# Kernel optimization log

Hardware: AMD Instinct MI355X
Metric: run time of the kernel (lower is better)

The kernel has to match this reference:

```python
import jax, jax.numpy as jnp
import numpy as np

B, S, D = 2, 2048, 2048
H, KVH, HD = 16, 4, 128
REP = H // KVH  # 4
THETA = 10000.0


def setup_inputs() -> dict:
    key = jax.random.key(0)
    ks = jax.random.split(key, 5)
    scale = 0.02
    x = jax.random.normal(ks[0], (B, S, D), dtype=jnp.float32)
    Wq = jax.random.normal(ks[1], (D, H * HD), dtype=jnp.float32) * scale
    Wk = jax.random.normal(ks[2], (D, KVH * HD), dtype=jnp.float32) * scale
    Wv = jax.random.normal(ks[3], (D, KVH * HD), dtype=jnp.float32) * scale
    Wo = jax.random.normal(ks[4], (H * HD, D), dtype=jnp.float32) * scale
    return {"x": x, "Wq": Wq, "Wk": Wk, "Wv": Wv, "Wo": Wo}


def _rope_cos_sin(seq_len, dtype):
    # HF-style rotary embedding: inv_freq over even dims, duplicated halves
    inv_freq = 1.0 / (THETA ** (jnp.arange(0, HD, 2, dtype=jnp.float32) / HD))
    pos = jnp.arange(seq_len, dtype=jnp.float32)
    ang = pos[:, None] * inv_freq[None, :]          # [S, HD/2]
    emb = jnp.concatenate([ang, ang], axis=-1)       # [S, HD]
    return jnp.cos(emb).astype(dtype), jnp.sin(emb).astype(dtype)


def _rotate_half(t):
    t1, t2 = jnp.split(t, 2, axis=-1)
    return jnp.concatenate([-t2, t1], axis=-1)


def reference(x, Wq, Wk, Wv, Wo):
    bsz, seq_len, _ = x.shape
    q = (x @ Wq).reshape(bsz, seq_len, H, HD).transpose(0, 2, 1, 3)    # [B,H,S,HD]
    k = (x @ Wk).reshape(bsz, seq_len, KVH, HD).transpose(0, 2, 1, 3)  # [B,KVH,S,HD]
    v = (x @ Wv).reshape(bsz, seq_len, KVH, HD).transpose(0, 2, 1, 3)
    cos, sin = _rope_cos_sin(seq_len, q.dtype)       # [S,HD]
    cos = cos[None, None, :, :]
    sin = sin[None, None, :, :]
    q = q * cos + _rotate_half(q) * sin
    k = k * cos + _rotate_half(k) * sin
    # repeat_interleave KV heads to match Q heads
    k = jnp.repeat(k, REP, axis=1)                   # [B,H,S,HD]
    v = jnp.repeat(v, REP, axis=1)
    scores = jnp.einsum('bhqd,bhkd->bhqk', q, k) / jnp.sqrt(jnp.float32(HD)).astype(q.dtype)
    i = jnp.arange(seq_len)
    causal = jnp.where(i[None, :] > i[:, None], jnp.float32(-jnp.inf), 0.0).astype(scores.dtype)
    scores = scores + causal[None, None, :, :]
    probs = jax.nn.softmax(scores.astype(jnp.float32), axis=-1).astype(q.dtype)
    out = jnp.einsum('bhqk,bhkd->bhqd', probs, v)    # [B,H,S,HD]
    out = out.transpose(0, 2, 1, 3).reshape(bsz, seq_len, H * HD)
    return out @ Wo
```

## Files before the change

### kernel.cpp

```cpp
#include <hip/hip_runtime.h>
#include <math.h>

#define B_   2
#define S_   2048
#define D_   2048
#define H_   16
#define KVH_ 4
#define HD_  128
#define REP_ 4

typedef __attribute__((ext_vector_type(8))) short bf16x8;
typedef __attribute__((ext_vector_type(4))) short bf16x4;
typedef __attribute__((ext_vector_type(4))) float f32x4;

#define QSCALE_LOG2E 0.1275266977097153f

__device__ __forceinline__ unsigned short f2bf(float x) {
    union { float f; unsigned u; } v; v.f = x;
    unsigned r = v.u + 0x7FFF + ((v.u >> 16) & 1);
    return (unsigned short)(r >> 16);
}

__device__ __forceinline__ unsigned short f2bf_fast(float x) {
    union { float f; unsigned u; } v; v.f = x;
    return (unsigned short)((v.u + 0x8000) >> 16);
}

__device__ __forceinline__ void gl_lds16(const unsigned short* g, unsigned short* l) {
    __builtin_amdgcn_global_load_lds(
        (const __attribute__((address_space(1))) unsigned int*)g,
        (__attribute__((address_space(3))) unsigned int*)l,
        16, 0, 0);
}

#define PH_BAR() do { asm volatile("" ::: "memory"); \
                      __builtin_amdgcn_s_barrier();  \
                      asm volatile("" ::: "memory"); } while (0)
#define VMW6 asm volatile("s_waitcnt vmcnt(6)" ::: "memory")
#define VMW4 asm volatile("s_waitcnt vmcnt(4)" ::: "memory")
#define VMW0 asm volatile("s_waitcnt vmcnt(0)" ::: "memory")

__global__ void cast_bf16(const float* __restrict__ src,
                          unsigned short* __restrict__ dst, int n4)
{
    int i = blockIdx.x * 256 + threadIdx.x;
    if (i >= n4) return;
    float4 v = *(const float4*)&src[(size_t)i * 4];
    bf16x4 o;
    o[0] = (short)f2bf(v.x); o[1] = (short)f2bf(v.y);
    o[2] = (short)f2bf(v.z); o[3] = (short)f2bf(v.w);
    *(bf16x4*)&dst[(size_t)i * 4] = o;
}

__global__ __launch_bounds__(256) void cast_transpose_all(
    const float* __restrict__ Wq, const float* __restrict__ Wk,
    const float* __restrict__ Wv, const float* __restrict__ Wo,
    unsigned short* __restrict__ Wqt, unsigned short* __restrict__ Wkt,
    unsigned short* __restrict__ Wvt, unsigned short* __restrict__ Wot)
{
    __shared__ float T[32][33];
    const int y = blockIdx.y;
    const float* src; unsigned short* dst; int C, bj;
    if (y < 64)      { src = Wq; dst = Wqt; C = 2048; bj = y; }
    else if (y < 80) { src = Wk; dst = Wkt; C = 512;  bj = y - 64; }
    else if (y < 96) { src = Wv; dst = Wvt; C = 512;  bj = y - 80; }
    else             { src = Wo; dst = Wot; C = 2048; bj = y - 96; }

    const int bi = blockIdx.x;
    const int t  = threadIdx.x;
    const int r  = t >> 3, cq = (t & 7) * 4;

    float4 v = *(const float4*)&src[(size_t)(bi * 32 + r) * C + bj * 32 + cq];
    T[r][cq + 0] = v.x; T[r][cq + 1] = v.y;
    T[r][cq + 2] = v.z; T[r][cq + 3] = v.w;
    __syncthreads();

    bf16x4 o;
    o[0] = (short)f2bf(T[cq + 0][r]);
    o[1] = (short)f2bf(T[cq + 1][r]);
    o[2] = (short)f2bf(T[cq + 2][r]);
    o[3] = (short)f2bf(T[cq + 3][r]);
    *(bf16x4*)&dst[(size_t)(bj * 32 + r) * 2048 + bi * 32 + cq] = o;
}

__global__ __launch_bounds__(512, 2) void qkv_mfma8(
    const unsigned short* __restrict__ Ah,
    const unsigned short* __restrict__ Wqt,
    const unsigned short* __restrict__ Wkt,
    const unsigned short* __restrict__ Wvt,
    unsigned short* __restrict__ Qh, unsigned short* __restrict__ Kh,
    unsigned short* __restrict__ Vt)
{
    __shared__ __align__(16) unsigned short lds[65536];

    const int bid = blockIdx.x;
    const int swz = (bid & 7) * 24 + (bid >> 3);
    const int bm = swz / 12, bn = swz % 12;
    const int m0 = bm * 256, n0 = bn * 256;

    const int tid  = threadIdx.x;
    const int w    = tid >> 6;
    const int lane = tid & 63;
    const int lo16 = lane & 15, quad = lane >> 4;
    const int wm   = w >> 2, wn = w & 3;

    const unsigned short* Bt;
    if (n0 < 2048)      Bt = Wqt + (size_t)n0 * 2048;
    else if (n0 < 2560) Bt = Wkt + (size_t)(n0 - 2048) * 2048;
    else                Bt = Wvt + (size_t)(n0 - 2560) * 2048;
    const unsigned short* Ag   = Ah + (size_t)m0 * 2048;
    const unsigned short* AgH1 = Ag + (size_t)128 * 2048;
    const unsigned short* BtH1 = Bt + (size_t)128 * 2048;

    const int rs   = lane >> 3;
    const int sce  = (((lane & 7) ^ rs) << 3);
    const int grow = w * 8 + rs;

    #define STAGE(gb, k0, lb) do {                                          \
        const unsigned short* _g = (gb) + (size_t)grow * 2048 + (k0) + sce; \
        gl_lds16(_g,                     (lb) + w * 512);                   \
        gl_lds16(_g + (size_t)64 * 2048, (lb) + (8 + w) * 512);             \
    } while (0)

    const int swb = (lo16 & 7) << 4;
    const int ac0 = (quad << 4) ^ swb;
    const int ac1 = (64 | (quad << 4)) ^ swb;
    char* ldsb = (char*)lds;
    const int abase = (wm * 128 + lo16) * 128;
    const int bbase = (wn * 16 + lo16) * 128 + 32768;

    f32x4 acc[8][4];
    #pragma unroll
    for (int mf = 0; mf < 8; ++mf)
        #pragma unroll
        for (int j = 0; j < 4; ++j) acc[mf][j] = (f32x4){0.f, 0.f, 0.f, 0.f};

    bf16x8 a0[4][2], a1[4][2], b0[2][2], b1[2][2];

    #define MM(Aa, Bb, mo, jo)                                               \
        _Pragma("unroll") for (int mf = 0; mf < 4; ++mf)                     \
        _Pragma("unroll") for (int j = 0; j < 2; ++j) {                      \
            acc[(mo)+mf][(jo)+j] = __builtin_amdgcn_mfma_f32_16x16x32_bf16(  \
                Aa[mf][0], Bb[j][0], acc[(mo)+mf][(jo)+j], 0, 0, 0);         \
            acc[(mo)+mf][(jo)+j] = __builtin_amdgcn_mfma_f32_16x16x32_bf16(  \
                Aa[mf][1], Bb[j][1], acc[(mo)+mf][(jo)+j], 0, 0, 0);         \
        }

    STAGE(Bt,   0,  lds + 16384);
    STAGE(BtH1, 0,  lds + 24576);
    STAGE(Ag,   0,  lds + 0);
    STAGE(AgH1, 0,  lds + 8192);
    STAGE(Bt,   64, lds + 32768 + 16384);
    STAGE(BtH1, 64, lds + 32768 + 24576);
    STAGE(Ag,   64, lds + 32768);
    VMW6;
    PH_BAR();

    #define PHASES(p, t)                                                         \
    {   _Pragma("unroll") for (int mf = 0; mf < 4; ++mf) {                       \
            a0[mf][0] = *(const bf16x8*)(ldsb + (p)*65536 + abase + mf*2048 + ac0); \
            a0[mf][1] = *(const bf16x8*)(ldsb + (p)*65536 + abase + mf*2048 + ac1); \
        }                                                                        \
        _Pragma("unroll") for (int j = 0; j < 2; ++j) {                          \
            b0[j][0] = *(const bf16x8*)(ldsb + (p)*65536 + bbase + j*8192 + ac0); \
            b0[j][1] = *(const bf16x8*)(ldsb + (p)*65536 + bbase + j*8192 + ac1); \
        }                                                                        \
        STAGE(AgH1, ((t)+1)*64, lds + ((p)^1)*32768 + 8192);                     \
        PH_BAR(); __builtin_amdgcn_s_setprio(1);                                 \
        MM(a0, b0, 0, 0);                                                        \
        __builtin_amdgcn_s_setprio(0); PH_BAR();                                 \
        _Pragma("unroll") for (int j = 0; j < 2; ++j) {                          \
            b1[j][0] = *(const bf16x8*)(ldsb + (p)*65536 + bbase + (j+2)*8192 + ac0); \
            b1[j][1] = *(const bf16x8*)(ldsb + (p)*65536 + bbase + (j+2)*8192 + ac1); \
        }                                                                        \
        STAGE(Bt, ((t)+2)*64, lds + (p)*32768 + 16384);                          \
        PH_BAR(); __builtin_amdgcn_s_setprio(1);                                 \
        MM(a0, b1, 0, 2);                                                        \
        __builtin_amdgcn_s_setprio(0); PH_BAR();                                 \
        _Pragma("unroll") for (int mf = 0; mf < 4; ++mf) {                       \
            a1[mf][0] = *(const bf16x8*)(ldsb + (p)*65536 + abase + (mf+4)*2048 + ac0); \
            a1[mf][1] = *(const bf16x8*)(ldsb + (p)*65536 + abase + (mf+4)*2048 + ac1); \
        }                                                                        \
        STAGE(BtH1, ((t)+2)*64, lds + (p)*32768 + 24576);                        \
        PH_BAR(); __builtin_amdgcn_s_setprio(1);                                 \
        MM(a1, b0, 4, 0);                                                        \
        __builtin_amdgcn_s_setprio(0); PH_BAR();                                 \
        STAGE(Ag, ((t)+2)*64, lds + (p)*32768);                                  \
        PH_BAR(); __builtin_amdgcn_s_setprio(1);                                 \
        MM(a1, b1, 4, 2);                                                        \
        __builtin_amdgcn_s_setprio(0);                                           \
        VMW6;                                                                    \
        PH_BAR();                                                                \
    }

    for (int it = 0; it < 16; ++it) {
        const int t = 2 * it;
        PHASES(0, t);
        PHASES(1, t + 1);
    }

    VMW0;
    PH_BAR();

    const int bb = m0 >> 11;
    const int s0loc = m0 & 2047;

    if (n0 < 2560) {
        const bool isQ = (n0 < 2048);
        const int h0 = isQ ? (n0 >> 7) : ((n0 - 2048) >> 7);
        const float post = isQ ? QSCALE_LOG2E : 1.0f;
        unsigned short* db[2];
        #pragma unroll
        for (int hp = 0; hp < 2; ++hp)
            db[hp] = isQ
                ? Qh + (((size_t)bb * H_   + h0 + hp) * S_) * HD_
                : Kh + (((size_t)bb * KVH_ + h0 + hp) * S_) * HD_;
        const int d = wn * 16 + lo16;
        const float inv = exp2f(-(float)d * 0.20761871093344086f);
        #pragma unroll
        for (int mf = 0; mf < 8; ++mf) {
            #pragma unroll
            for (int r = 0; r < 4; ++r) {
                int s = s0loc + wm * 128 + mf * 16 + quad * 4 + r;
                float sn, c;
                sincosf((float)s * inv, &sn, &c);
                #pragma unroll
                for (int hp = 0; hp < 2; ++hp) {
                    float lo = acc[mf][2 * hp + 0][r];
                    float hi = acc[mf][2 * hp + 1][r];
                    unsigned short* drow = db[hp] + (size_t)s * HD_;
                    drow[d]      = f2bf((lo * c - hi * sn) * post);
                    drow[d + 64] = f2bf((hi * c + lo * sn) * post);
                }
            }
        }
    } else {
        const int g0 = (n0 - 2560) >> 7;
        unsigned short* Ts = lds;
        const int d = wn * 16 + lo16;
        #pragma unroll
        for (int hp = 0; hp < 2; ++hp) {
            if (hp) PH_BAR();
            #pragma unroll
            for (int mf = 0; mf < 8; ++mf) {
                int ml = wm * 128 + mf * 16 + quad * 4;
                bf16x4 v0, v1;
                #pragma unroll
                for (int r = 0; r < 4; ++r) {
                    v0[r] = (short)f2bf(acc[mf][2 * hp + 0][r]);
                    v1[r] = (short)f2bf(acc[mf][2 * hp + 1][r]);
                }
                *(bf16x4*)&Ts[(size_t)d        * 264 + ml] = v0;
                *(bf16x4*)&Ts[(size_t)(d + 64) * 264 + ml] = v1;
            }
            PH_BAR();
            unsigned short* dstb = Vt + (((size_t)bb * KVH_ + g0 + hp) * HD_) * S_ + s0loc;
            #pragma unroll
            for (int itb = 0; itb < 8; ++itb) {
                int dd = itb * 16 + (tid >> 5);
                int ch = (tid & 31) * 8;
                *(bf16x8*)(dstb + (size_t)dd * S_ + ch) =
                    *(const bf16x8*)&Ts[(size_t)dd * 264 + ch];
            }
        }
    }
    #undef PHASES
    #undef MM
    #undef STAGE
}

__global__ __launch_bounds__(512, 4) void flash_attn_mfma(
    const unsigned short* __restrict__ Qh,
    const unsigned short* __restrict__ Kh,
    const unsigned short* __restrict__ Vt,
    unsigned short* __restrict__ attb)
{
    const int bh   = blockIdx.x;
    const int yy   = blockIdx.y;
    const int qt   = (yy < 8) ? (15 - yy) : (yy - 8);
    const int b    = bh >> 4, h = bh & 15;
    const int g    = h >> 2;
    const int tid  = threadIdx.x;
    const int w    = tid >> 6;
    const int lane = tid & 63;
    const int lo16 = lane & 15;
    const int quad = lane >> 4;

    const unsigned short* Qb = Qh + (((size_t)b * H_   + h) * S_) * HD_;
    const unsigned short* Kb = Kh + (((size_t)b * KVH_ + g) * S_) * HD_;
    const unsigned short* Vb = Vt + (((size_t)b * KVH_ + g) * HD_) * S_;

    __shared__ __align__(16) unsigned short Ks[64][136];
    __shared__ __align__(16) unsigned short Vs[128][72];
    __shared__ __align__(16) unsigned short Ps[8][16][72];

    const int q0 = qt * 128;
    const int qw = q0 + w * 16;

    bf16x8 qf[4];
    #pragma unroll
    for (int kc = 0; kc < 4; ++kc)
        qf[kc] = *(const bf16x8*)(Qb + (size_t)(qw + lo16) * HD_ + kc * 32 + quad * 8);

    f32x4 o[8];
    #pragma unroll
    for (int n = 0; n < 8; ++n) o[n] = (f32x4){0.f, 0.f, 0.f, 0.f};
    float l_loc[4];
    #pragma unroll
    for (int r = 0; r < 4; ++r) l_loc[r] = 0.0f;

    const int kr  = tid >> 4, kcu = tid & 15;
    const int vr  = tid >> 3, vcu = tid & 7;

    bf16x8 kreg[2], vreg[2];
    #pragma unroll
    for (int i = 0; i < 2; ++i) {
        kreg[i] = *(const bf16x8*)(Kb + (size_t)(32 * i + kr) * HD_ + kcu * 8);
        vreg[i] = *(const bf16x8*)(Vb + (size_t)(64 * i + vr) * S_ + vcu * 8);
    }

    const int ktend = 2 * qt + 1;
    for (int kt = 0; kt <= ktend; ++kt) {
        const int k0 = kt * 64;
        asm volatile("s_barrier" ::: "memory");
        #pragma unroll
        for (int i = 0; i < 2; ++i) {
            *(bf16x8*)&Ks[32 * i + kr][kcu * 8] = kreg[i];
            *(bf16x8*)&Vs[64 * i + vr][vcu * 8] = vreg[i];
        }
        if (kt < ktend) {
            const int k0n = k0 + 64;
            #pragma unroll
            for (int i = 0; i < 2; ++i) {
                kreg[i] = *(const bf16x8*)(Kb + (size_t)(k0n + 32 * i + kr) * HD_ + kcu * 8);
                vreg[i] = *(const bf16x8*)(Vb + (size_t)(64 * i + vr) * S_ + k0n + vcu * 8);
            }
        }
        asm volatile("s_waitcnt lgkmcnt(0)" ::: "memory");
        asm volatile("s_barrier" ::: "memory");

        if (w >= 4 || kt < ktend) {
            f32x4 sc[4];
            #pragma unroll
            for (int cb = 0; cb < 4; ++cb) sc[cb] = (f32x4){0.f, 0.f, 0.f, 0.f};
            #pragma unroll
            for (int kc = 0; kc < 4; ++kc)
                #pragma unroll
                for (int cb = 0; cb < 4; ++cb) {
                    bf16x8 kf = *(const bf16x8*)&Ks[cb * 16 + lo16][kc * 32 + quad * 8];
                    sc[cb] = __builtin_amdgcn_mfma_f32_16x16x32_bf16(
                        qf[kc], kf, sc[cb], 0, 0, 0);
                }

            const bool masked = (w < 4) ? (kt == 2 * qt) : (kt == ktend);
            if (masked) {
                #pragma unroll
                for (int r = 0; r < 4; ++r) {
                    const int row = qw + quad * 4 + r;
                    float lacc = 0.0f;
                    #pragma unroll
                    for (int cb = 0; cb < 4; ++cb) {
                        float xv = sc[cb][r];
                        if ((k0 + cb * 16 + lo16) > row) xv = -1e30f;
                        float p = exp2f(xv);
                        lacc += p;
                        Ps[w][quad * 4 + r][cb * 16 + lo16] = f2bf_fast(p);
                    }
                    l_loc[r] += lacc;
                }
            } else {
                #pragma unroll
                for (int r = 0; r < 4; ++r) {
                    float lacc = 0.0f;
                    #pragma unroll
                    for (int cb = 0; cb < 4; ++cb) {
                        float p = exp2f(sc[cb][r]);
                        lacc += p;
                        Ps[w][quad * 4 + r][cb * 16 + lo16] = f2bf_fast(p);
                    }
                    l_loc[r] += lacc;
                }
            }

            #pragma unroll
            for (int kc = 0; kc < 2; ++kc) {
                bf16x8 pf = *(const bf16x8*)&Ps[w][lo16][kc * 32 + quad * 8];
                #pragma unroll
                for (int n = 0; n < 8; ++n) {
                    bf16x8 vf = *(const bf16x8*)&Vs[n * 16 + lo16][kc * 32 + quad * 8];
                    o[n] = __builtin_amdgcn_mfma_f32_16x16x32_bf16(
                        pf, vf, o[n], 0, 0, 0);
                }
            }
        }
    }

    #pragma unroll
    for (int r = 0; r < 4; ++r) {
        float l = l_loc[r];
        l += __shfl_xor(l, 1);
        l += __shfl_xor(l, 2);
        l += __shfl_xor(l, 4);
        l += __shfl_xor(l, 8);
        float invl = 1.0f / l;
        int srow = qw + quad * 4 + r;
        unsigned short* dst = attb + ((size_t)b * S_ + srow) * D_ + h * HD_;
        #pragma unroll
        for (int n = 0; n < 8; ++n)
            dst[n * 16 + lo16] = f2bf(o[n][r] * invl);
    }
}

__global__ __launch_bounds__(512, 2) void out_mfma8(
    const unsigned short* __restrict__ Ah,
    const unsigned short* __restrict__ Wot,
    float* __restrict__ C)
{
    __shared__ __align__(16) unsigned short lds[49152];

    const int bid = blockIdx.x;
    const int swz = (bid & 7) * 32 + (bid >> 3);
    const int bm = swz >> 4, bn = swz & 15;
    const int m0 = bm * 256, n0 = bn * 128;

    const int tid  = threadIdx.x;
    const int w    = tid >> 6;
    const int lane = tid & 63;
    const int lo16 = lane & 15, quad = lane >> 4;
    const int wm   = w >> 2, wn = w & 3;

    const unsigned short* Ag   = Ah  + (size_t)m0 * 2048;
    const unsigned short* AgH1 = Ag  + (size_t)128 * 2048;
    const unsigned short* Bt   = Wot + (size_t)n0 * 2048;

    const int rs   = lane >> 3;
    const int sce  = (((lane & 7) ^ rs) << 3);
    const int grow = w * 8 + rs;

    #define OSTAGE(gb, k0, lb) do {                                         \
        const unsigned short* _g = (gb) + (size_t)grow * 2048 + (k0) + sce; \
        gl_lds16(_g,                     (lb) + w * 512);                   \
        gl_lds16(_g + (size_t)64 * 2048, (lb) + (8 + w) * 512);             \
    } while (0)

    const int swb = (lo16 & 7) << 4;
    const int ac0 = (quad << 4) ^ swb;
    const int ac1 = (64 | (quad << 4)) ^ swb;
    char* ldsb = (char*)lds;
    const int abase = (wm * 128 + lo16) * 128;
    const int bbase = (wn * 32 + lo16) * 128 + 32768;

    f32x4 acc[8][2];
    #pragma unroll
    for (int mf = 0; mf < 8; ++mf)
        #pragma unroll
        for (int j = 0; j < 2; ++j) acc[mf][j] = (f32x4){0.f, 0.f, 0.f, 0.f};

    bf16x8 a0[4][2], a1[4][2], bb[2][2];

    #define OMM(Aa, mo, j)                                                   \
        _Pragma("unroll") for (int mf = 0; mf < 4; ++mf) {                   \
            acc[(mo)+mf][j] = __builtin_amdgcn_mfma_f32_16x16x32_bf16(       \
                Aa[mf][0], bb[j][0], acc[(mo)+mf][j], 0, 0, 0);              \
            acc[(mo)+mf][j] = __builtin_amdgcn_mfma_f32_16x16x32_bf16(       \
                Aa[mf][1], bb[j][1], acc[(mo)+mf][j], 0, 0, 0);              \
        }

    OSTAGE(Bt,   0,  lds + 16384);
    OSTAGE(Ag,   0,  lds + 0);
    OSTAGE(AgH1, 0,  lds + 8192);
    OSTAGE(Bt,   64, lds + 24576 + 16384);
    OSTAGE(Ag,   64, lds + 24576);
    VMW4;
    PH_BAR();

    #define OPH(p, t)                                                            \
    {   _Pragma("unroll") for (int mf = 0; mf < 4; ++mf) {                       \
            a0[mf][0] = *(const bf16x8*)(ldsb + (p)*49152 + abase + mf*2048 + ac0); \
            a0[mf][1] = *(const bf16x8*)(ldsb + (p)*49152 + abase + mf*2048 + ac1); \
        }                                                                        \
        _Pragma("unroll") for (int j = 0; j < 2; ++j) {                          \
            bb[j][0] = *(const bf16x8*)(ldsb + (p)*49152 + bbase + j*2048 + ac0); \
            bb[j][1] = *(const bf16x8*)(ldsb + (p)*49152 + bbase + j*2048 + ac1); \
        }                                                                        \
        OSTAGE(AgH1, ((t)+1)*64, lds + ((p)^1)*24576 + 8192);                    \
        PH_BAR(); __builtin_amdgcn_s_setprio(1);                                 \
        OMM(a0, 0, 0);                                                           \
        __builtin_amdgcn_s_setprio(0); PH_BAR();                                 \
        OSTAGE(Bt, ((t)+2)*64, lds + (p)*24576 + 16384);                         \
        PH_BAR(); __builtin_amdgcn_s_setprio(1);                                 \
        OMM(a0, 0, 1);                                                           \
        __builtin_amdgcn_s_setprio(0); PH_BAR();                                 \
        _Pragma("unroll") for (int mf = 0; mf < 4; ++mf) {                       \
            a1[mf][0] = *(const bf16x8*)(ldsb + (p)*49152 + abase + (mf+4)*2048 + ac0); \
            a1[mf][1] = *(const bf16x8*)(ldsb + (p)*49152 + abase + (mf+4)*2048 + ac1); \
        }                                                                        \
        PH_BAR(); __builtin_amdgcn_s_setprio(1);                                 \
        OMM(a1, 4, 0);                                                           \
        __builtin_amdgcn_s_setprio(0); PH_BAR();                                 \
        OSTAGE(Ag, ((t)+2)*64, lds + (p)*24576);                                 \
        PH_BAR(); __builtin_amdgcn_s_setprio(1);                                 \
        OMM(a1, 4, 1);                                                           \
        __builtin_amdgcn_s_setprio(0);                                           \
        VMW4;                                                                    \
        PH_BAR();                                                                \
    }

    for (int it = 0; it < 16; ++it) {
        const int t = 2 * it;
        OPH(0, t);
        OPH(1, t + 1);
    }

    VMW0;

    #pragma unroll
    for (int mf = 0; mf < 8; ++mf)
        #pragma unroll
        for (int r = 0; r < 4; ++r) {
            size_t m = (size_t)(m0 + wm * 128 + mf * 16 + quad * 4 + r);
            #pragma unroll
            for (int j = 0; j < 2; ++j)
                C[m * 2048 + n0 + wn * 32 + j * 16 + lo16] = acc[mf][j][r];
        }
    #undef OPH
    #undef OMM
    #undef OSTAGE
}

extern "C" void kernel_launch(void* const* d_in, const int* in_sizes, int n_in,
                              void* d_out, int out_size, void* d_ws, size_t ws_size,
                              hipStream_t stream)
{
    const float* x  = (const float*)d_in[0];
    const float* Wq = (const float*)d_in[1];
    const float* Wk = (const float*)d_in[2];
    const float* Wv = (const float*)d_in[3];
    const float* Wo = (const float*)d_in[4];
    float* out = (float*)d_out;

    unsigned short* xh  = (unsigned short*)d_ws;
    unsigned short* Wqt = xh  + (size_t)4096 * 2048;
    unsigned short* Wkt = Wqt + (size_t)2048 * 2048;
    unsigned short* Wvt = Wkt + (size_t)512 * 2048;
    unsigned short* Wot = Wvt + (size_t)512 * 2048;
    unsigned short* Qh  = Wot + (size_t)2048 * 2048;
    unsigned short* Kh  = Qh  + (size_t)B_ * H_   * S_ * HD_;
    unsigned short* Vt  = Kh  + (size_t)B_ * KVH_ * S_ * HD_;
    unsigned short* attb= xh;

    cast_bf16<<<(4096 * 2048 / 4 + 255) / 256, 256, 0, stream>>>(x, xh, 4096 * 2048 / 4);
    cast_transpose_all<<<dim3(64, 160), 256, 0, stream>>>(Wq, Wk, Wv, Wo, Wqt, Wkt, Wvt, Wot);

    qkv_mfma8<<<192, 512, 0, stream>>>(xh, Wqt, Wkt, Wvt, Qh, Kh, Vt);

    flash_attn_mfma<<<dim3(32, 16), 512, 0, stream>>>(Qh, Kh, Vt, attb);

    out_mfma8<<<256, 512, 0, stream>>>(attb, Wot, out);
}
```

Before: 274.5 us.

## Double-buffer K/V tiles with XOR-swizzled LDS and transposed score MFMA

```diff
diff --git a/kernel.cpp b/kernel.cpp
--- a/kernel.cpp
+++ b/kernel.cpp
@@ -290,12 +290,14 @@
     const unsigned short* Kb = Kh + (((size_t)b * KVH_ + g) * S_) * HD_;
     const unsigned short* Vb = Vt + (((size_t)b * KVH_ + g) * HD_) * S_;
 
-    __shared__ __align__(16) unsigned short Ks[64][136];
-    __shared__ __align__(16) unsigned short Vs[128][72];
-    __shared__ __align__(16) unsigned short Ps[8][16][72];
-
-    const int q0 = qt * 128;
-    const int qw = q0 + w * 16;
+    __shared__ __align__(16) unsigned short Ks[2][64][128];
+    __shared__ __align__(16) unsigned short Vs[2][128][64];
+    __shared__ __align__(16) unsigned short Ps[8][16][64];
+
+    const int q0   = qt * 128;
+    const int qw   = q0 + w * 16;
+    const int rowq = qw + lo16;
+    const int rsw  = lo16 & 7;
 
     bf16x8 qf[4];
     #pragma unroll
@@ -305,41 +307,37 @@
     f32x4 o[8];
     #pragma unroll
     for (int n = 0; n < 8; ++n) o[n] = (f32x4){0.f, 0.f, 0.f, 0.f};
-    float l_loc[4];
-    #pragma unroll
-    for (int r = 0; r < 4; ++r) l_loc[r] = 0.0f;
-
-    const int kr  = tid >> 4, kcu = tid & 15;
-    const int vr  = tid >> 3, vcu = tid & 7;
+    float l_loc = 0.0f;
+
+    const int kr = tid >> 3, ku = tid & 7, kx = kr & 7;
+    const int vr = tid >> 2, vu = tid & 3, vx = vr & 7;
 
     bf16x8 kreg[2], vreg[2];
-    #pragma unroll
-    for (int i = 0; i < 2; ++i) {
-        kreg[i] = *(const bf16x8*)(Kb + (size_t)(32 * i + kr) * HD_ + kcu * 8);
-        vreg[i] = *(const bf16x8*)(Vb + (size_t)(64 * i + vr) * S_ + vcu * 8);
-    }
+    kreg[0] = *(const bf16x8*)(Kb + (size_t)kr * HD_ + ku * 8);
+    kreg[1] = *(const bf16x8*)(Kb + (size_t)kr * HD_ + (ku + 8) * 8);
+    vreg[0] = *(const bf16x8*)(Vb + (size_t)vr * S_ + vu * 8);
+    vreg[1] = *(const bf16x8*)(Vb + (size_t)vr * S_ + (vu + 4) * 8);
+    *(bf16x8*)&Ks[0][kr][(ku ^ kx) * 8]       = kreg[0];
+    *(bf16x8*)&Ks[0][kr][((ku + 8) ^ kx) * 8] = kreg[1];
+    *(bf16x8*)&Vs[0][vr][(vu ^ vx) * 8]       = vreg[0];
+    *(bf16x8*)&Vs[0][vr][((vu + 4) ^ vx) * 8] = vreg[1];
+    asm volatile("s_waitcnt lgkmcnt(0)" ::: "memory");
 
     const int ktend = 2 * qt + 1;
     for (int kt = 0; kt <= ktend; ++kt) {
-        const int k0 = kt * 64;
+        const int p = kt & 1;
         asm volatile("s_barrier" ::: "memory");
-        #pragma unroll
-        for (int i = 0; i < 2; ++i) {
-            *(bf16x8*)&Ks[32 * i + kr][kcu * 8] = kreg[i];
-            *(bf16x8*)&Vs[64 * i + vr][vcu * 8] = vreg[i];
-        }
+
         if (kt < ktend) {
-            const int k0n = k0 + 64;
-            #pragma unroll
-            for (int i = 0; i < 2; ++i) {
-                kreg[i] = *(const bf16x8*)(Kb + (size_t)(k0n + 32 * i + kr) * HD_ + kcu * 8);
-                vreg[i] = *(const bf16x8*)(Vb + (size_t)(64 * i + vr) * S_ + k0n + vcu * 8);
-            }
-        }
-        asm volatile("s_waitcnt lgkmcnt(0)" ::: "memory");
-        asm volatile("s_barrier" ::: "memory");
+            const int k0n = (kt + 1) * 64;
+            kreg[0] = *(const bf16x8*)(Kb + (size_t)(k0n + kr) * HD_ + ku * 8);
+            kreg[1] = *(const bf16x8*)(Kb + (size_t)(k0n + kr) * HD_ + (ku + 8) * 8);
+            vreg[0] = *(const bf16x8*)(Vb + (size_t)vr * S_ + k0n + vu * 8);
+            vreg[1] = *(const bf16x8*)(Vb + (size_t)vr * S_ + k0n + (vu + 4) * 8);
+        }
 
         if (w >= 4 || kt < ktend) {
+            const int k0 = kt * 64;
             f32x4 sc[4];
             #pragma unroll
             for (int cb = 0; cb < 4; ++cb) sc[cb] = (f32x4){0.f, 0.f, 0.f, 0.f};
@@ -347,62 +345,59 @@
             for (int kc = 0; kc < 4; ++kc)
                 #pragma unroll
                 for (int cb = 0; cb < 4; ++cb) {
-                    bf16x8 kf = *(const bf16x8*)&Ks[cb * 16 + lo16][kc * 32 + quad * 8];
+                    bf16x8 kf = *(const bf16x8*)&Ks[p][cb * 16 + lo16]
+                                                   [((kc * 4 + quad) ^ rsw) * 8];
                     sc[cb] = __builtin_amdgcn_mfma_f32_16x16x32_bf16(
-                        qf[kc], kf, sc[cb], 0, 0, 0);
+                        kf, qf[kc], sc[cb], 0, 0, 0);
                 }
 
             const bool masked = (w < 4) ? (kt == 2 * qt) : (kt == ktend);
-            if (masked) {
+            const int kvb = k0 + quad * 4;
+            float lacc = 0.0f;
+            #pragma unroll
+            for (int cb = 0; cb < 4; ++cb) {
+                bf16x4 pk;
                 #pragma unroll
                 for (int r = 0; r < 4; ++r) {
-                    const int row = qw + quad * 4 + r;
-                    float lacc = 0.0f;
-                    #pragma unroll
-                    for (int cb = 0; cb < 4; ++cb) {
-                        float xv = sc[cb][r];
-                        if ((k0 + cb * 16 + lo16) > row) xv = -1e30f;
-                        float p = exp2f(xv);
-                        lacc += p;
-                        Ps[w][quad * 4 + r][cb * 16 + lo16] = f2bf_fast(p);
-                    }
-                    l_loc[r] += lacc;
+                    float xv = sc[cb][r];
+                    if (masked && (kvb + cb * 16 + r) > rowq) xv = -1e30f;
+                    float pp = exp2f(xv);
+                    lacc += pp;
+                    pk[r] = (short)f2bf_fast(pp);
                 }
-            } else {
-                #pragma unroll
-                for (int r = 0; r < 4; ++r) {
-                    float lacc = 0.0f;
-                    #pragma unroll
-                    for (int cb = 0; cb < 4; ++cb) {
-                        float p = exp2f(sc[cb][r]);
-                        lacc += p;
-                        Ps[w][quad * 4 + r][cb * 16 + lo16] = f2bf_fast(p);
-                    }
-                    l_loc[r] += lacc;
-                }
+                *(bf16x4*)&Ps[w][lo16][(((cb * 2 + (quad >> 1)) ^ rsw) * 8
+                                         + (quad & 1) * 4)] = pk;
             }
+            l_loc += lacc;
 
             #pragma unroll
             for (int kc = 0; kc < 2; ++kc) {
-                bf16x8 pf = *(const bf16x8*)&Ps[w][lo16][kc * 32 + quad * 8];
+                bf16x8 pf = *(const bf16x8*)&Ps[w][lo16][((kc * 4 + quad) ^ rsw) * 8];
                 #pragma unroll
                 for (int n = 0; n < 8; ++n) {
-                    bf16x8 vf = *(const bf16x8*)&Vs[n * 16 + lo16][kc * 32 + quad * 8];
+                    bf16x8 vf = *(const bf16x8*)&Vs[p][n * 16 + lo16]
+                                                   [((kc * 4 + quad) ^ rsw) * 8];
                     o[n] = __builtin_amdgcn_mfma_f32_16x16x32_bf16(
                         pf, vf, o[n], 0, 0, 0);
                 }
             }
         }
-    }
-
+
+        if (kt < ktend) {
+            *(bf16x8*)&Ks[p ^ 1][kr][(ku ^ kx) * 8]       = kreg[0];
+            *(bf16x8*)&Ks[p ^ 1][kr][((ku + 8) ^ kx) * 8] = kreg[1];
+            *(bf16x8*)&Vs[p ^ 1][vr][(vu ^ vx) * 8]       = vreg[0];
+            *(bf16x8*)&Vs[p ^ 1][vr][((vu + 4) ^ vx) * 8] = vreg[1];
+        }
+        asm volatile("s_waitcnt lgkmcnt(0)" ::: "memory");
+    }
+
+    float l = l_loc;
+    l += __shfl_xor(l, 16);
+    l += __shfl_xor(l, 32);
     #pragma unroll
     for (int r = 0; r < 4; ++r) {
-        float l = l_loc[r];
-        l += __shfl_xor(l, 1);
-        l += __shfl_xor(l, 2);
-        l += __shfl_xor(l, 4);
-        l += __shfl_xor(l, 8);
-        float invl = 1.0f / l;
+        float invl = 1.0f / __shfl(l, quad * 4 + r);
         int srow = qw + quad * 4 + r;
         unsigned short* dst = attb + ((size_t)b * S_ + srow) * D_ + h * HD_;
         #pragma unroll
```

Result: slower. 291.4 us (+6.1%).

## Double-buffer K/V tiles and compute next QK^T scores one step ahead

Applied to the files above, without the earlier changes.

```diff
diff --git a/kernel.cpp b/kernel.cpp
--- a/kernel.cpp
+++ b/kernel.cpp
@@ -290,8 +290,8 @@
     const unsigned short* Kb = Kh + (((size_t)b * KVH_ + g) * S_) * HD_;
     const unsigned short* Vb = Vt + (((size_t)b * KVH_ + g) * HD_) * S_;
 
-    __shared__ __align__(16) unsigned short Ks[64][136];
-    __shared__ __align__(16) unsigned short Vs[128][72];
+    __shared__ __align__(16) unsigned short Ks[2][64][136];
+    __shared__ __align__(16) unsigned short Vs[2][128][72];
     __shared__ __align__(16) unsigned short Ps[8][16][72];
 
     const int q0 = qt * 128;
@@ -313,45 +313,71 @@
     const int vr  = tid >> 3, vcu = tid & 7;
 
     bf16x8 kreg[2], vreg[2];
+
     #pragma unroll
     for (int i = 0; i < 2; ++i) {
         kreg[i] = *(const bf16x8*)(Kb + (size_t)(32 * i + kr) * HD_ + kcu * 8);
         vreg[i] = *(const bf16x8*)(Vb + (size_t)(64 * i + vr) * S_ + vcu * 8);
     }
+    #pragma unroll
+    for (int i = 0; i < 2; ++i) {
+        *(bf16x8*)&Ks[0][32 * i + kr][kcu * 8] = kreg[i];
+        *(bf16x8*)&Vs[0][64 * i + vr][vcu * 8] = vreg[i];
+    }
+    #pragma unroll
+    for (int i = 0; i < 2; ++i) {
+        kreg[i] = *(const bf16x8*)(Kb + (size_t)(64 + 32 * i + kr) * HD_ + kcu * 8);
+        vreg[i] = *(const bf16x8*)(Vb + (size_t)(64 * i + vr) * S_ + 64 + vcu * 8);
+    }
+    #pragma unroll
+    for (int i = 0; i < 2; ++i) {
+        *(bf16x8*)&Ks[1][32 * i + kr][kcu * 8] = kreg[i];
+        *(bf16x8*)&Vs[1][64 * i + vr][vcu * 8] = vreg[i];
+    }
+    asm volatile("s_waitcnt lgkmcnt(0)" ::: "memory");
+    asm volatile("s_barrier" ::: "memory");
+
+    f32x4 scC[4];
+    #pragma unroll
+    for (int cb = 0; cb < 4; ++cb) scC[cb] = (f32x4){0.f, 0.f, 0.f, 0.f};
+    #pragma unroll
+    for (int kc = 0; kc < 4; ++kc)
+        #pragma unroll
+        for (int cb = 0; cb < 4; ++cb) {
+            bf16x8 kf = *(const bf16x8*)&Ks[0][cb * 16 + lo16][kc * 32 + quad * 8];
+            scC[cb] = __builtin_amdgcn_mfma_f32_16x16x32_bf16(
+                qf[kc], kf, scC[cb], 0, 0, 0);
+        }
 
     const int ktend = 2 * qt + 1;
     for (int kt = 0; kt <= ktend; ++kt) {
-        const int k0 = kt * 64;
-        asm volatile("s_barrier" ::: "memory");
-        #pragma unroll
-        for (int i = 0; i < 2; ++i) {
-            *(bf16x8*)&Ks[32 * i + kr][kcu * 8] = kreg[i];
-            *(bf16x8*)&Vs[64 * i + vr][vcu * 8] = vreg[i];
-        }
+        const int p = kt & 1;
+
+        f32x4 scN[4];
+        #pragma unroll
+        for (int cb = 0; cb < 4; ++cb) scN[cb] = (f32x4){0.f, 0.f, 0.f, 0.f};
         if (kt < ktend) {
-            const int k0n = k0 + 64;
+            #pragma unroll
+            for (int kc = 0; kc < 4; ++kc)
+                #pragma unroll
+                for (int cb = 0; cb < 4; ++cb) {
+                    bf16x8 kf = *(const bf16x8*)&Ks[p ^ 1][cb * 16 + lo16][kc * 32 + quad * 8];
+                    scN[cb] = __builtin_amdgcn_mfma_f32_16x16x32_bf16(
+                        qf[kc], kf, scN[cb], 0, 0, 0);
+                }
+        }
+
+        if (kt + 2 <= ktend) {
+            const int k0n = (kt + 2) * 64;
             #pragma unroll
             for (int i = 0; i < 2; ++i) {
                 kreg[i] = *(const bf16x8*)(Kb + (size_t)(k0n + 32 * i + kr) * HD_ + kcu * 8);
                 vreg[i] = *(const bf16x8*)(Vb + (size_t)(64 * i + vr) * S_ + k0n + vcu * 8);
             }
         }
-        asm volatile("s_waitcnt lgkmcnt(0)" ::: "memory");
-        asm volatile("s_barrier" ::: "memory");
 
         if (w >= 4 || kt < ktend) {
-            f32x4 sc[4];
-            #pragma unroll
-            for (int cb = 0; cb < 4; ++cb) sc[cb] = (f32x4){0.f, 0.f, 0.f, 0.f};
-            #pragma unroll
-            for (int kc = 0; kc < 4; ++kc)
-                #pragma unroll
-                for (int cb = 0; cb < 4; ++cb) {
-                    bf16x8 kf = *(const bf16x8*)&Ks[cb * 16 + lo16][kc * 32 + quad * 8];
-                    sc[cb] = __builtin_amdgcn_mfma_f32_16x16x32_bf16(
-                        qf[kc], kf, sc[cb], 0, 0, 0);
-                }
-
+            const int k0 = kt * 64;
             const bool masked = (w < 4) ? (kt == 2 * qt) : (kt == ktend);
             if (masked) {
                 #pragma unroll
@@ -360,11 +386,11 @@
                     float lacc = 0.0f;
                     #pragma unroll
                     for (int cb = 0; cb < 4; ++cb) {
-                        float xv = sc[cb][r];
+                        float xv = scC[cb][r];
                         if ((k0 + cb * 16 + lo16) > row) xv = -1e30f;
-                        float p = exp2f(xv);
-                        lacc += p;
-                        Ps[w][quad * 4 + r][cb * 16 + lo16] = f2bf_fast(p);
+                        float pp = exp2f(xv);
+                        lacc += pp;
+                        Ps[w][quad * 4 + r][cb * 16 + lo16] = f2bf_fast(pp);
                     }
                     l_loc[r] += lacc;
                 }
@@ -374,9 +400,9 @@
                     float lacc = 0.0f;
                     #pragma unroll
                     for (int cb = 0; cb < 4; ++cb) {
-                        float p = exp2f(sc[cb][r]);
-                        lacc += p;
-                        Ps[w][quad * 4 + r][cb * 16 + lo16] = f2bf_fast(p);
+                        float pp = exp2f(scC[cb][r]);
+                        lacc += pp;
+                        Ps[w][quad * 4 + r][cb * 16 + lo16] = f2bf_fast(pp);
                     }
                     l_loc[r] += lacc;
                 }
@@ -387,12 +413,26 @@
                 bf16x8 pf = *(const bf16x8*)&Ps[w][lo16][kc * 32 + quad * 8];
                 #pragma unroll
                 for (int n = 0; n < 8; ++n) {
-                    bf16x8 vf = *(const bf16x8*)&Vs[n * 16 + lo16][kc * 32 + quad * 8];
+                    bf16x8 vf = *(const bf16x8*)&Vs[p][n * 16 + lo16][kc * 32 + quad * 8];
                     o[n] = __builtin_amdgcn_mfma_f32_16x16x32_bf16(
                         pf, vf, o[n], 0, 0, 0);
                 }
             }
         }
+
+        asm volatile("s_barrier" ::: "memory");
+        if (kt + 2 <= ktend) {
+            #pragma unroll
+            for (int i = 0; i < 2; ++i) {
+                *(bf16x8*)&Ks[p][32 * i + kr][kcu * 8] = kreg[i];
+                *(bf16x8*)&Vs[p][64 * i + vr][vcu * 8] = vreg[i];
+            }
+        }
+        asm volatile("s_waitcnt lgkmcnt(0)" ::: "memory");
+        asm volatile("s_barrier" ::: "memory");
+
+        #pragma unroll
+        for (int cb = 0; cb < 4; ++cb) scC[cb] = scN[cb];
     }
 
     #pragma unroll
```

Result: slower. 298.5 us (+8.7%).

## Retile QKV GEMM to 128x384 tiles for 256 blocks

Applied to the files above, without the earlier changes.

```diff
diff --git a/kernel.cpp b/kernel.cpp
--- a/kernel.cpp
+++ b/kernel.cpp
@@ -83,7 +83,7 @@
     *(bf16x4*)&dst[(size_t)(bj * 32 + r) * 2048 + bi * 32 + cq] = o;
 }
 
-__global__ __launch_bounds__(512, 2) void qkv_mfma8(
+__global__ __launch_bounds__(512, 2) void qkv_mfma12(
     const unsigned short* __restrict__ Ah,
     const unsigned short* __restrict__ Wqt,
     const unsigned short* __restrict__ Wkt,
@@ -94,9 +94,9 @@
     __shared__ __align__(16) unsigned short lds[65536];
 
     const int bid = blockIdx.x;
-    const int swz = (bid & 7) * 24 + (bid >> 3);
-    const int bm = swz / 12, bn = swz % 12;
-    const int m0 = bm * 256, n0 = bn * 256;
+    const int swz = (bid & 7) * 32 + (bid >> 3);
+    const int bn = swz >> 5, bm = swz & 31;
+    const int m0 = bm * 128, n0 = bn * 384;
 
     const int tid  = threadIdx.x;
     const int w    = tid >> 6;
@@ -104,13 +104,11 @@
     const int lo16 = lane & 15, quad = lane >> 4;
     const int wm   = w >> 2, wn = w & 3;
 
-    const unsigned short* Bt;
-    if (n0 < 2048)      Bt = Wqt + (size_t)n0 * 2048;
-    else if (n0 < 2560) Bt = Wkt + (size_t)(n0 - 2048) * 2048;
-    else                Bt = Wvt + (size_t)(n0 - 2560) * 2048;
+    const unsigned short* Wall = Wqt;
+    const unsigned short* Bt   = Wall + (size_t)n0 * 2048;
+    const unsigned short* B1g  = Bt + (size_t)128 * 2048;
+    const unsigned short* B2g  = Bt + (size_t)256 * 2048;
     const unsigned short* Ag   = Ah + (size_t)m0 * 2048;
-    const unsigned short* AgH1 = Ag + (size_t)128 * 2048;
-    const unsigned short* BtH1 = Bt + (size_t)128 * 2048;
 
     const int rs   = lane >> 3;
     const int sce  = (((lane & 7) ^ rs) << 3);
@@ -126,68 +124,60 @@
     const int ac0 = (quad << 4) ^ swb;
     const int ac1 = (64 | (quad << 4)) ^ swb;
     char* ldsb = (char*)lds;
-    const int abase = (wm * 128 + lo16) * 128;
-    const int bbase = (wn * 16 + lo16) * 128 + 32768;
-
-    f32x4 acc[8][4];
-    #pragma unroll
-    for (int mf = 0; mf < 8; ++mf)
+    const int abase = (wm * 64 + lo16) * 128;
+
+    f32x4 acc[4][6];
+    #pragma unroll
+    for (int mf = 0; mf < 4; ++mf)
         #pragma unroll
-        for (int j = 0; j < 4; ++j) acc[mf][j] = (f32x4){0.f, 0.f, 0.f, 0.f};
-
-    bf16x8 a0[4][2], a1[4][2], b0[2][2], b1[2][2];
-
-    #define MM(Aa, Bb, mo, jo)                                               \
+        for (int j = 0; j < 6; ++j) acc[mf][j] = (f32x4){0.f, 0.f, 0.f, 0.f};
+
+    bf16x8 af[4][2], bf[3][2][2];
+
+    #define MMG(g)                                                           \
         _Pragma("unroll") for (int mf = 0; mf < 4; ++mf)                     \
-        _Pragma("unroll") for (int j = 0; j < 2; ++j) {                      \
-            acc[(mo)+mf][(jo)+j] = __builtin_amdgcn_mfma_f32_16x16x32_bf16(  \
-                Aa[mf][0], Bb[j][0], acc[(mo)+mf][(jo)+j], 0, 0, 0);         \
-            acc[(mo)+mf][(jo)+j] = __builtin_amdgcn_mfma_f32_16x16x32_bf16(  \
-                Aa[mf][1], Bb[j][1], acc[(mo)+mf][(jo)+j], 0, 0, 0);         \
-        }
-
-    STAGE(Bt,   0,  lds + 16384);
-    STAGE(BtH1, 0,  lds + 24576);
-    STAGE(Ag,   0,  lds + 0);
-    STAGE(AgH1, 0,  lds + 8192);
-    STAGE(Bt,   64, lds + 32768 + 16384);
-    STAGE(BtH1, 64, lds + 32768 + 24576);
-    STAGE(Ag,   64, lds + 32768);
+        _Pragma("unroll") for (int jj = 0; jj < 2; ++jj) {                   \
+            acc[mf][2*(g)+jj] = __builtin_amdgcn_mfma_f32_16x16x32_bf16(     \
+                af[mf][0], bf[g][jj][0], acc[mf][2*(g)+jj], 0, 0, 0);        \
+            acc[mf][2*(g)+jj] = __builtin_amdgcn_mfma_f32_16x16x32_bf16(     \
+                af[mf][1], bf[g][jj][1], acc[mf][2*(g)+jj], 0, 0, 0);        \
+        }
+
+    STAGE(Bt,  0, lds + 8192);
+    STAGE(B1g, 0, lds + 16384);
+    STAGE(B2g, 0, lds + 24576);
+    STAGE(Ag,  0, lds + 0);
+    STAGE(Bt,  64, lds + 32768 + 8192);
+    STAGE(B1g, 64, lds + 32768 + 16384);
+    STAGE(B2g, 64, lds + 32768 + 24576);
     VMW6;
     PH_BAR();
 
-    #define PHASES(p, t)                                                         \
+    #define QPH(p, t)                                                            \
     {   _Pragma("unroll") for (int mf = 0; mf < 4; ++mf) {                       \
-            a0[mf][0] = *(const bf16x8*)(ldsb + (p)*65536 + abase + mf*2048 + ac0); \
-            a0[mf][1] = *(const bf16x8*)(ldsb + (p)*65536 + abase + mf*2048 + ac1); \
+            af[mf][0] = *(const bf16x8*)(ldsb + (p)*65536 + abase + mf*2048 + ac0); \
+            af[mf][1] = *(const bf16x8*)(ldsb + (p)*65536 + abase + mf*2048 + ac1); \
         }                                                                        \
-        _Pragma("unroll") for (int j = 0; j < 2; ++j) {                          \
-            b0[j][0] = *(const bf16x8*)(ldsb + (p)*65536 + bbase + j*8192 + ac0); \
-            b0[j][1] = *(const bf16x8*)(ldsb + (p)*65536 + bbase + j*8192 + ac1); \
+        _Pragma("unroll") for (int g = 0; g < 3; ++g)                            \
+        _Pragma("unroll") for (int jj = 0; jj < 2; ++jj) {                       \
+            const int f = g * 8 + wn + jj * 4;                                   \
+            bf[g][jj][0] = *(const bf16x8*)(ldsb + (p)*65536 + 16384             \
+                                            + (f*16 + lo16)*128 + ac0);          \
+            bf[g][jj][1] = *(const bf16x8*)(ldsb + (p)*65536 + 16384             \
+                                            + (f*16 + lo16)*128 + ac1);          \
         }                                                                        \
-        STAGE(AgH1, ((t)+1)*64, lds + ((p)^1)*32768 + 8192);                     \
-        PH_BAR(); __builtin_amdgcn_s_setprio(1);                                 \
-        MM(a0, b0, 0, 0);                                                        \
+        STAGE(Ag, ((t)+1)*64, lds + ((p)^1)*32768);                              \
+        PH_BAR(); __builtin_amdgcn_s_setprio(1);                                 \
+        MMG(0);                                                                  \
         __builtin_amdgcn_s_setprio(0); PH_BAR();                                 \
-        _Pragma("unroll") for (int j = 0; j < 2; ++j) {                          \
-            b1[j][0] = *(const bf16x8*)(ldsb + (p)*65536 + bbase + (j+2)*8192 + ac0); \
-            b1[j][1] = *(const bf16x8*)(ldsb + (p)*65536 + bbase + (j+2)*8192 + ac1); \
-        }                                                                        \
-        STAGE(Bt, ((t)+2)*64, lds + (p)*32768 + 16384);                          \
-        PH_BAR(); __builtin_amdgcn_s_setprio(1);                                 \
-        MM(a0, b1, 0, 2);                                                        \
+        STAGE(Bt, ((t)+2)*64, lds + (p)*32768 + 8192);                           \
+        PH_BAR(); __builtin_amdgcn_s_setprio(1);                                 \
+        MMG(1);                                                                  \
         __builtin_amdgcn_s_setprio(0); PH_BAR();                                 \
-        _Pragma("unroll") for (int mf = 0; mf < 4; ++mf) {                       \
-            a1[mf][0] = *(const bf16x8*)(ldsb + (p)*65536 + abase + (mf+4)*2048 + ac0); \
-            a1[mf][1] = *(const bf16x8*)(ldsb + (p)*65536 + abase + (mf+4)*2048 + ac1); \
-        }                                                                        \
-        STAGE(BtH1, ((t)+2)*64, lds + (p)*32768 + 24576);                        \
-        PH_BAR(); __builtin_amdgcn_s_setprio(1);                                 \
-        MM(a1, b0, 4, 0);                                                        \
-        __builtin_amdgcn_s_setprio(0); PH_BAR();                                 \
-        STAGE(Ag, ((t)+2)*64, lds + (p)*32768);                                  \
-        PH_BAR(); __builtin_amdgcn_s_setprio(1);                                 \
-        MM(a1, b1, 4, 2);                                                        \
+        STAGE(B1g, ((t)+2)*64, lds + (p)*32768 + 16384);                         \
+        STAGE(B2g, ((t)+2)*64, lds + (p)*32768 + 24576);                         \
+        PH_BAR(); __builtin_amdgcn_s_setprio(1);                                 \
+        MMG(2);                                                                  \
         __builtin_amdgcn_s_setprio(0);                                           \
         VMW6;                                                                    \
         PH_BAR();                                                                \
@@ -195,8 +185,8 @@
 
     for (int it = 0; it < 16; ++it) {
         const int t = 2 * it;
-        PHASES(0, t);
-        PHASES(1, t + 1);
+        QPH(0, t);
+        QPH(1, t + 1);
     }
 
     VMW0;
@@ -204,68 +194,61 @@
 
     const int bb = m0 >> 11;
     const int s0loc = m0 & 2047;
-
-    if (n0 < 2560) {
-        const bool isQ = (n0 < 2048);
-        const int h0 = isQ ? (n0 >> 7) : ((n0 - 2048) >> 7);
-        const float post = isQ ? QSCALE_LOG2E : 1.0f;
-        unsigned short* db[2];
-        #pragma unroll
-        for (int hp = 0; hp < 2; ++hp)
-            db[hp] = isQ
-                ? Qh + (((size_t)bb * H_   + h0 + hp) * S_) * HD_
-                : Kh + (((size_t)bb * KVH_ + h0 + hp) * S_) * HD_;
-        const int d = wn * 16 + lo16;
-        const float inv = exp2f(-(float)d * 0.20761871093344086f);
-        #pragma unroll
-        for (int mf = 0; mf < 8; ++mf) {
-            #pragma unroll
-            for (int r = 0; r < 4; ++r) {
-                int s = s0loc + wm * 128 + mf * 16 + quad * 4 + r;
-                float sn, c;
-                sincosf((float)s * inv, &sn, &c);
+    const int d = wn * 16 + lo16;
+    const float inv = exp2f(-(float)d * 0.20761871093344086f);
+    unsigned short* Ts = lds;
+
+    #pragma unroll
+    for (int g = 0; g < 3; ++g) {
+        const int cg = n0 + g * 128;
+        if (cg < 2560) {
+            const bool isQ = (cg < 2048);
+            const float post = isQ ? QSCALE_LOG2E : 1.0f;
+            unsigned short* dstb = isQ
+                ? Qh + (((size_t)bb * H_   + (cg >> 7))          * S_) * HD_
+                : Kh + (((size_t)bb * KVH_ + ((cg - 2048) >> 7)) * S_) * HD_;
+            #pragma unroll
+            for (int mf = 0; mf < 4; ++mf) {
                 #pragma unroll
-                for (int hp = 0; hp < 2; ++hp) {
-                    float lo = acc[mf][2 * hp + 0][r];
-                    float hi = acc[mf][2 * hp + 1][r];
-                    unsigned short* drow = db[hp] + (size_t)s * HD_;
+                for (int r = 0; r < 4; ++r) {
+                    int s = s0loc + wm * 64 + mf * 16 + quad * 4 + r;
+                    float sn, c;
+                    sincosf((float)s * inv, &sn, &c);
+                    float lo = acc[mf][2 * g + 0][r];
+                    float hi = acc[mf][2 * g + 1][r];
+                    unsigned short* drow = dstb + (size_t)s * HD_;
                     drow[d]      = f2bf((lo * c - hi * sn) * post);
                     drow[d + 64] = f2bf((hi * c + lo * sn) * post);
                 }
             }
-        }
-    } else {
-        const int g0 = (n0 - 2560) >> 7;
-        unsigned short* Ts = lds;
-        const int d = wn * 16 + lo16;
-        #pragma unroll
-        for (int hp = 0; hp < 2; ++hp) {
-            if (hp) PH_BAR();
-            #pragma unroll
-            for (int mf = 0; mf < 8; ++mf) {
-                int ml = wm * 128 + mf * 16 + quad * 4;
+        } else {
+            const int g0 = (cg - 2560) >> 7;
+            PH_BAR();
+            #pragma unroll
+            for (int mf = 0; mf < 4; ++mf) {
+                int ml = wm * 64 + mf * 16 + quad * 4;
                 bf16x4 v0, v1;
                 #pragma unroll
                 for (int r = 0; r < 4; ++r) {
-                    v0[r] = (short)f2bf(acc[mf][2 * hp + 0][r]);
-                    v1[r] = (short)f2bf(acc[mf][2 * hp + 1][r]);
+                    v0[r] = (short)f2bf(acc[mf][2 * g + 0][r]);
+                    v1[r] = (short)f2bf(acc[mf][2 * g + 1][r]);
                 }
-                *(bf16x4*)&Ts[(size_t)d        * 264 + ml] = v0;
-                *(bf16x4*)&Ts[(size_t)(d + 64) * 264 + ml] = v1;
+                *(bf16x4*)&Ts[(size_t)d        * 136 + ml] = v0;
+                *(bf16x4*)&Ts[(size_t)(d + 64) * 136 + ml] = v1;
             }
             PH_BAR();
-            unsigned short* dstb = Vt + (((size_t)bb * KVH_ + g0 + hp) * HD_) * S_ + s0loc;
-            #pragma unroll
-            for (int itb = 0; itb < 8; ++itb) {
-                int dd = itb * 16 + (tid >> 5);
-                int ch = (tid & 31) * 8;
+            unsigned short* dstb = Vt + (((size_t)bb * KVH_ + g0) * HD_) * S_ + s0loc;
+            #pragma unroll
+            for (int itb = 0; itb < 4; ++itb) {
+                int dd = itb * 32 + (tid >> 4);
+                int ch = (tid & 15) * 8;
                 *(bf16x8*)(dstb + (size_t)dd * S_ + ch) =
-                    *(const bf16x8*)&Ts[(size_t)dd * 264 + ch];
+                    *(const bf16x8*)&Ts[(size_t)dd * 136 + ch];
             }
         }
     }
-    #undef PHASES
-    #undef MM
+    #undef QPH
+    #undef MMG
     #undef STAGE
 }
 
@@ -552,7 +535,7 @@
     cast_bf16<<<(4096 * 2048 / 4 + 255) / 256, 256, 0, stream>>>(x, xh, 4096 * 2048 / 4);
     cast_transpose_all<<<dim3(64, 160), 256, 0, stream>>>(Wq, Wk, Wv, Wo, Wqt, Wkt, Wvt, Wot);
 
-    qkv_mfma8<<<192, 512, 0, stream>>>(xh, Wqt, Wkt, Wvt, Qh, Kh, Vt);
+    qkv_mfma12<<<256, 512, 0, stream>>>(xh, Wqt, Wkt, Wvt, Qh, Kh, Vt);
 
     flash_attn_mfma<<<dim3(32, 16), 512, 0, stream>>>(Qh, Kh, Vt, attb);
 
```

Result: no change. 272.6 us (-0.7%).
